# Kernel tuning notes

Measured on AMD Instinct MI355X. Metric: run time of the kernel, lower is better.

## Reference

```python
import jax, jax.numpy as jnp
import numpy as np

N_NODES = 50000
N_EDGES = 800000
F_IN = 128
F_OUT = 64
ALPHA = 0.2  # LeakyReLU negative slope


def setup_inputs() -> dict:
    key = jax.random.key(0)
    k1, k2, k3, k4, k5, k6 = jax.random.split(key, 6)
    inp = jax.random.normal(k1, (N_NODES, F_IN), dtype=jnp.float32)
    W = jax.random.normal(k2, (F_IN, F_OUT), dtype=jnp.float32) * 0.05
    a = jax.random.normal(k3, (1, 2 * F_OUT), dtype=jnp.float32) * 0.05
    adj_vals = jax.random.uniform(k4, (N_EDGES,), dtype=jnp.float32)
    src = jax.random.randint(k5, (N_EDGES,), 0, N_NODES)
    dst = jax.random.randint(k6, (N_EDGES,), 0, N_NODES)
    edge_index = jnp.stack([src, dst], axis=0).astype(jnp.int64)
    return {"input": inp, "W": W, "a": a, "adj_vals": adj_vals, "edge_index": edge_index}


def reference(input, W, a, adj_vals, edge_index):
    N = input.shape[0]
    src, dst = edge_index[0], edge_index[1]
    # h = input @ W  (dropout is identity in eval mode)
    h = input @ W  # (N, F_OUT)
    # a.mm(edge_h) with edge_h = [h[src]; h[dst]] decomposes into two per-node dots
    a_src, a_dst = a[0, :F_OUT], a[0, F_OUT:]
    score_src = h @ a_src  # (N,)
    score_dst = h @ a_dst  # (N,)
    scores = score_src[src] + score_dst[dst]  # (E,)
    edge_e = jnp.exp(-jax.nn.leaky_relu(scores, ALPHA)) * adj_vals  # (E,)
    # sparse spmm: row-sum normalizer and weighted aggregation over neighbors
    e_rowsum = jax.ops.segment_sum(edge_e, src, num_segments=N)  # (N,)
    h_prime = jax.ops.segment_sum(edge_e[:, None] * h[dst], src, num_segments=N)  # (N, F_OUT)
    h_prime = h_prime / e_rowsum[:, None]
    return jax.nn.elu(h_prime)  # concat=True
```

## Files before the change

### kernel.cpp

```cpp
#include <hip/hip_runtime.h>
#include <math.h>

#define N_NODES 50000
#define N_EDGES 800000
#define F_IN    128
#define F_OUT   64
#define ALPHA   0.2f

#define NP      50176
#define NB      196

__global__ __launch_bounds__(256) void k_gemm_scores(
    const float* __restrict__ in, const float* __restrict__ W,
    const float* __restrict__ a, float* __restrict__ h,
    float* __restrict__ ssrc, float* __restrict__ sdst) {
  __shared__ float Wl[F_IN * F_OUT];
  __shared__ float al[2 * F_OUT];

  for (int i = threadIdx.x; i < F_IN * F_OUT; i += 256) Wl[i] = W[i];
  if (threadIdx.x < 2 * F_OUT) al[threadIdx.x] = a[threadIdx.x];
  __syncthreads();

  const int wave = threadIdx.x >> 6;
  const int lane = threadIdx.x & 63;
  const int wgrp = blockIdx.x * 4 + wave;
  if (wgrp >= N_NODES / 8) return;
  const int row0 = wgrp * 8;

  const float* rb = in + (size_t)row0 * F_IN;
  float acc[8] = {0.f, 0.f, 0.f, 0.f, 0.f, 0.f, 0.f, 0.f};

  #pragma unroll 4
  for (int k4 = 0; k4 < F_IN / 4; ++k4) {
    float4 iv[8];
    #pragma unroll
    for (int r = 0; r < 8; ++r)
      iv[r] = *reinterpret_cast<const float4*>(rb + (size_t)r * F_IN + k4 * 4);
    #pragma unroll
    for (int j = 0; j < 4; ++j) {
      const float w = Wl[(k4 * 4 + j) * F_OUT + lane];
      #pragma unroll
      for (int r = 0; r < 8; ++r)
        acc[r] += (&iv[r].x)[j] * w;
    }
  }

  #pragma unroll
  for (int r = 0; r < 8; ++r)
    h[(size_t)(row0 + r) * F_OUT + lane] = acc[r];

  const float as = al[lane], ad = al[F_OUT + lane];
  float ts[8], td[8];
  #pragma unroll
  for (int r = 0; r < 8; ++r) { ts[r] = acc[r] * as; td[r] = acc[r] * ad; }
  #pragma unroll
  for (int off = 32; off; off >>= 1) {
    #pragma unroll
    for (int r = 0; r < 8; ++r) {
      ts[r] += __shfl_xor(ts[r], off);
      td[r] += __shfl_xor(td[r], off);
    }
  }
  if (lane == 0) {
    #pragma unroll
    for (int r = 0; r < 8; ++r) {
      ssrc[row0 + r] = ts[r];
      sdst[row0 + r] = td[r];
    }
  }
}

__global__ __launch_bounds__(256) void k_hist(const int* __restrict__ src,
                                              int* __restrict__ deg) {
  const int e = blockIdx.x * 256 + threadIdx.x;
  atomicAdd(&deg[src[e]], 1);
}

__global__ __launch_bounds__(256) void k_scan_a(const int* __restrict__ deg,
                                                int* __restrict__ offs,
                                                int* __restrict__ bsum) {
  __shared__ int lds[256];
  const int i = blockIdx.x * 256 + threadIdx.x;
  const int v = deg[i];
  lds[threadIdx.x] = v;
  __syncthreads();
  #pragma unroll
  for (int off = 1; off < 256; off <<= 1) {
    int t = (threadIdx.x >= off) ? lds[threadIdx.x - off] : 0;
    __syncthreads();
    lds[threadIdx.x] += t;
    __syncthreads();
  }
  offs[i] = lds[threadIdx.x] - v;
  if (threadIdx.x == 255) bsum[blockIdx.x] = lds[255];
}

__global__ __launch_bounds__(256) void k_scan_b(const int* __restrict__ bsum,
                                                int* __restrict__ boff) {
  __shared__ int lds[256];
  const int v = (threadIdx.x < NB) ? bsum[threadIdx.x] : 0;
  lds[threadIdx.x] = v;
  __syncthreads();
  #pragma unroll
  for (int off = 1; off < 256; off <<= 1) {
    int t = (threadIdx.x >= off) ? lds[threadIdx.x - off] : 0;
    __syncthreads();
    lds[threadIdx.x] += t;
    __syncthreads();
  }
  boff[threadIdx.x] = lds[threadIdx.x] - v;
}

__global__ __launch_bounds__(256) void k_scatter(
    const int* __restrict__ src, const int* __restrict__ dst,
    const float* __restrict__ adj,
    const float* __restrict__ ssrc, const float* __restrict__ sdst,
    const int* __restrict__ offs, const int* __restrict__ boff,
    int* __restrict__ cursor, int2* __restrict__ pairs) {
  const int e = blockIdx.x * 256 + threadIdx.x;
  const int s = src[e];
  const int d = dst[e];
  const float sc = ssrc[s] + sdst[d];
  const float lr = sc > 0.f ? sc : ALPHA * sc;
  const float ee = expf(-lr) * adj[e];
  const int base = offs[s] + boff[s >> 8];
  const int pos  = base + atomicAdd(&cursor[s], 1);
  pairs[pos] = make_int2(d, __float_as_int(ee));
}

__global__ __launch_bounds__(256) void k_gather(
    const int2* __restrict__ pairs, const int* __restrict__ offs,
    const int* __restrict__ boff, const float* __restrict__ h,
    float* __restrict__ out) {
  const int wave = threadIdx.x >> 6;
  const int lane = threadIdx.x & 63;
  const int node = blockIdx.x * 4 + wave;

  const int o0 = offs[node] + boff[node >> 8];
  const int o1 = offs[node + 1] + boff[(node + 1) >> 8];

  float acc = 0.f, rs = 0.f;
  int j = o0;
  for (; j + 3 < o1; j += 4) {
    const int2 p0 = pairs[j];
    const int2 p1 = pairs[j + 1];
    const int2 p2 = pairs[j + 2];
    const int2 p3 = pairs[j + 3];
    const float h0 = h[(size_t)p0.x * F_OUT + lane];
    const float h1 = h[(size_t)p1.x * F_OUT + lane];
    const float h2 = h[(size_t)p2.x * F_OUT + lane];
    const float h3 = h[(size_t)p3.x * F_OUT + lane];
    const float e0 = __int_as_float(p0.y);
    const float e1 = __int_as_float(p1.y);
    const float e2 = __int_as_float(p2.y);
    const float e3 = __int_as_float(p3.y);
    acc += e0 * h0; rs += e0;
    acc += e1 * h1; rs += e1;
    acc += e2 * h2; rs += e2;
    acc += e3 * h3; rs += e3;
  }
  for (; j < o1; ++j) {
    const int2 p = pairs[j];
    const float ee = __int_as_float(p.y);
    acc += ee * h[(size_t)p.x * F_OUT + lane];
    rs  += ee;
  }

  float v = acc / rs;
  v = v > 0.f ? v : expm1f(v);
  out[(size_t)node * F_OUT + lane] = v;
}

extern "C" void kernel_launch(void* const* d_in, const int* in_sizes, int n_in,
                              void* d_out, int out_size, void* d_ws, size_t ws_size,
                              hipStream_t stream) {
  const float* input = (const float*)d_in[0];
  const float* W     = (const float*)d_in[1];
  const float* a     = (const float*)d_in[2];
  const float* adj   = (const float*)d_in[3];
  const int*   ei    = (const int*)d_in[4];
  const int*   src   = ei;
  const int*   dst   = ei + N_EDGES;
  float* out = (float*)d_out;

  float* h    = (float*)d_ws;
  float* ssrc = h + (size_t)N_NODES * F_OUT;
  float* sdst = ssrc + N_NODES;
  int*   deg    = (int*)(sdst + N_NODES);
  int*   cursor = deg + NP;
  int*   offs   = cursor + NP;
  int*   bsum   = offs + NP;
  int*   boff   = bsum + 256;
  int2*  pairs  = (int2*)(boff + 256);

  hipMemsetAsync(deg, 0, 2 * NP * sizeof(int), stream);

  k_hist   <<<N_EDGES / 256, 256, 0, stream>>>(src, deg);
  k_scan_a <<<NB, 256, 0, stream>>>(deg, offs, bsum);
  k_scan_b <<<1, 256, 0, stream>>>(bsum, boff);
  k_gemm_scores<<<(N_NODES / 8 + 3) / 4, 256, 0, stream>>>(input, W, a, h, ssrc, sdst);
  k_scatter<<<N_EDGES / 256, 256, 0, stream>>>(src, dst, adj, ssrc, sdst,
                                               offs, boff, cursor, pairs);
  k_gather <<<N_NODES / 4, 256, 0, stream>>>(pairs, offs, boff, h, out);
}
```

Before: 260.7 us.

## Compute one node row per thread with transposed W read via broadcast loads

The GEMM now has each thread own one full input row (32 float4 held in registers) and compute all 64 outputs and both attention scores itself, which removes the LDS staging of W and the cross-lane shuffle reductions. W is transposed into workspace by an extra block added to the histogram kernel, so every lane reads the same W address (a uniform, cache-friendly broadcast). The cost is heavy register use (128 floats for the row), which lowers occupancy, and only 196 blocks are launched. Each thread also reads a strided 512-byte row, which makes input loads uncoalesced.

```diff
diff --git a/kernel.cpp b/kernel.cpp
--- a/kernel.cpp
+++ b/kernel.cpp
@@ -11,67 +11,67 @@
 #define NB      196
 
 __global__ __launch_bounds__(256) void k_gemm_scores(
-    const float* __restrict__ in, const float* __restrict__ W,
+    const float* __restrict__ in, const float* __restrict__ Wt,
     const float* __restrict__ a, float* __restrict__ h,
     float* __restrict__ ssrc, float* __restrict__ sdst) {
-  __shared__ float Wl[F_IN * F_OUT];
-  __shared__ float al[2 * F_OUT];
-
-  for (int i = threadIdx.x; i < F_IN * F_OUT; i += 256) Wl[i] = W[i];
-  if (threadIdx.x < 2 * F_OUT) al[threadIdx.x] = a[threadIdx.x];
-  __syncthreads();
-
+  const int lane = threadIdx.x & 63;
   const int wave = threadIdx.x >> 6;
-  const int lane = threadIdx.x & 63;
-  const int wgrp = blockIdx.x * 4 + wave;
-  if (wgrp >= N_NODES / 8) return;
-  const int row0 = wgrp * 8;
-
-  const float* rb = in + (size_t)row0 * F_IN;
-  float acc[8] = {0.f, 0.f, 0.f, 0.f, 0.f, 0.f, 0.f, 0.f};
-
-  #pragma unroll 4
-  for (int k4 = 0; k4 < F_IN / 4; ++k4) {
-    float4 iv[8];
+  const int row  = (blockIdx.x * 4 + wave) * 64 + lane;
+  const int rl   = row < N_NODES ? row : N_NODES - 1;
+
+  float4 ar[32];
+  const float4* rp = reinterpret_cast<const float4*>(in + (size_t)rl * F_IN);
+  #pragma unroll
+  for (int i = 0; i < 32; ++i) ar[i] = rp[i];
+
+  float ss = 0.f, sd = 0.f;
+  const bool live = (row < N_NODES);
+
+  for (int g = 0; g < 16; ++g) {
+    const float4* w0 = reinterpret_cast<const float4*>(Wt + (size_t)(g * 4 + 0) * F_IN);
+    const float4* w1 = reinterpret_cast<const float4*>(Wt + (size_t)(g * 4 + 1) * F_IN);
+    const float4* w2 = reinterpret_cast<const float4*>(Wt + (size_t)(g * 4 + 2) * F_IN);
+    const float4* w3 = reinterpret_cast<const float4*>(Wt + (size_t)(g * 4 + 3) * F_IN);
+    float a0 = 0.f, a1 = 0.f, a2 = 0.f, a3 = 0.f;
     #pragma unroll
-    for (int r = 0; r < 8; ++r)
-      iv[r] = *reinterpret_cast<const float4*>(rb + (size_t)r * F_IN + k4 * 4);
-    #pragma unroll
-    for (int j = 0; j < 4; ++j) {
-      const float w = Wl[(k4 * 4 + j) * F_OUT + lane];
-      #pragma unroll
-      for (int r = 0; r < 8; ++r)
-        acc[r] += (&iv[r].x)[j] * w;
+    for (int kb = 0; kb < 32; ++kb) {
+      const float4 r  = ar[kb];
+      const float4 v0 = w0[kb];
+      const float4 v1 = w1[kb];
+      const float4 v2 = w2[kb];
+      const float4 v3 = w3[kb];
+      a0 = fmaf(r.x, v0.x, a0); a0 = fmaf(r.y, v0.y, a0);
+      a0 = fmaf(r.z, v0.z, a0); a0 = fmaf(r.w, v0.w, a0);
+      a1 = fmaf(r.x, v1.x, a1); a1 = fmaf(r.y, v1.y, a1);
+      a1 = fmaf(r.z, v1.z, a1); a1 = fmaf(r.w, v1.w, a1);
+      a2 = fmaf(r.x, v2.x, a2); a2 = fmaf(r.y, v2.y, a2);
+      a2 = fmaf(r.z, v2.z, a2); a2 = fmaf(r.w, v2.w, a2);
+      a3 = fmaf(r.x, v3.x, a3); a3 = fmaf(r.y, v3.y, a3);
+      a3 = fmaf(r.z, v3.z, a3); a3 = fmaf(r.w, v3.w, a3);
     }
-  }
-
-  #pragma unroll
-  for (int r = 0; r < 8; ++r)
-    h[(size_t)(row0 + r) * F_OUT + lane] = acc[r];
-
-  const float as = al[lane], ad = al[F_OUT + lane];
-  float ts[8], td[8];
-  #pragma unroll
-  for (int r = 0; r < 8; ++r) { ts[r] = acc[r] * as; td[r] = acc[r] * ad; }
-  #pragma unroll
-  for (int off = 32; off; off >>= 1) {
-    #pragma unroll
-    for (int r = 0; r < 8; ++r) {
-      ts[r] += __shfl_xor(ts[r], off);
-      td[r] += __shfl_xor(td[r], off);
+    ss += a0 * a[g * 4 + 0] + a1 * a[g * 4 + 1]
+        + a2 * a[g * 4 + 2] + a3 * a[g * 4 + 3];
+    sd += a0 * a[F_OUT + g * 4 + 0] + a1 * a[F_OUT + g * 4 + 1]
+        + a2 * a[F_OUT + g * 4 + 2] + a3 * a[F_OUT + g * 4 + 3];
+    if (live) {
+      float4 hv = make_float4(a0, a1, a2, a3);
+      reinterpret_cast<float4*>(h + (size_t)row * F_OUT)[g] = hv;
     }
   }
-  if (lane == 0) {
-    #pragma unroll
-    for (int r = 0; r < 8; ++r) {
-      ssrc[row0 + r] = ts[r];
-      sdst[row0 + r] = td[r];
+  if (live) { ssrc[row] = ss; sdst[row] = sd; }
+}
+
+__global__ __launch_bounds__(256) void k_hist(const int* __restrict__ src,
+                                              int* __restrict__ deg,
+                                              const float* __restrict__ W,
+                                              float* __restrict__ Wt) {
+  if (blockIdx.x == N_EDGES / 256) {
+    for (int i = threadIdx.x; i < F_IN * F_OUT; i += 256) {
+      const int k = i >> 6, j = i & 63;
+      Wt[j * F_IN + k] = W[i];
     }
-  }
-}
-
-__global__ __launch_bounds__(256) void k_hist(const int* __restrict__ src,
-                                              int* __restrict__ deg) {
+    return;
+  }
   const int e = blockIdx.x * 256 + threadIdx.x;
   atomicAdd(&deg[src[e]], 1);
 }
@@ -191,14 +191,15 @@
   int*   offs   = cursor + NP;
   int*   bsum   = offs + NP;
   int*   boff   = bsum + 256;
-  int2*  pairs  = (int2*)(boff + 256);
+  float* Wt     = (float*)(boff + 256);
+  int2*  pairs  = (int2*)(Wt + F_IN * F_OUT);
 
   hipMemsetAsync(deg, 0, 2 * NP * sizeof(int), stream);
 
-  k_hist   <<<N_EDGES / 256, 256, 0, stream>>>(src, deg);
+  k_hist   <<<N_EDGES / 256 + 1, 256, 0, stream>>>(src, deg, W, Wt);
   k_scan_a <<<NB, 256, 0, stream>>>(deg, offs, bsum);
   k_scan_b <<<1, 256, 0, stream>>>(bsum, boff);
-  k_gemm_scores<<<(N_NODES / 8 + 3) / 4, 256, 0, stream>>>(input, W, a, h, ssrc, sdst);
+  k_gemm_scores<<<NB, 256, 0, stream>>>(input, Wt, a, h, ssrc, sdst);
   k_scatter<<<N_EDGES / 256, 256, 0, stream>>>(src, dst, adj, ssrc, sdst,
                                                offs, boff, cursor, pairs);
   k_gather <<<N_NODES / 4, 256, 0, stream>>>(pairs, offs, boff, h, out);
```

After: 303.5 us. 1.16x slower.

## Rewrite projection GEMM as 64-row LDS-tiled 4x4 register-blocked kernel

Applied to the files above, without the earlier changes.

Replaces the per-wave 8-row GEMM, in which each lane computed one output column, with a block-level 64x64 tile. The input tile is staged transposed into LDS, and each thread computes a 4x4 register block from float4 LDS reads. Score reductions now shuffle across 16 lanes. This is meant to raise arithmetic intensity and cut redundant global input loads, which the old scheme broadcast per lane. The cost is more LDS use (about 50KB per block), which may limit occupancy, and an extra sync per K-chunk.

```diff
diff --git a/kernel.cpp b/kernel.cpp
--- a/kernel.cpp
+++ b/kernel.cpp
@@ -14,58 +14,96 @@
     const float* __restrict__ in, const float* __restrict__ W,
     const float* __restrict__ a, float* __restrict__ h,
     float* __restrict__ ssrc, float* __restrict__ sdst) {
-  __shared__ float Wl[F_IN * F_OUT];
+  __shared__ float Ws[F_IN][F_OUT];
+  __shared__ float As[64][68];
   __shared__ float al[2 * F_OUT];
 
-  for (int i = threadIdx.x; i < F_IN * F_OUT; i += 256) Wl[i] = W[i];
-  if (threadIdx.x < 2 * F_OUT) al[threadIdx.x] = a[threadIdx.x];
-  __syncthreads();
-
-  const int wave = threadIdx.x >> 6;
-  const int lane = threadIdx.x & 63;
-  const int wgrp = blockIdx.x * 4 + wave;
-  if (wgrp >= N_NODES / 8) return;
-  const int row0 = wgrp * 8;
-
-  const float* rb = in + (size_t)row0 * F_IN;
-  float acc[8] = {0.f, 0.f, 0.f, 0.f, 0.f, 0.f, 0.f, 0.f};
-
-  #pragma unroll 4
-  for (int k4 = 0; k4 < F_IN / 4; ++k4) {
-    float4 iv[8];
-    #pragma unroll
-    for (int r = 0; r < 8; ++r)
-      iv[r] = *reinterpret_cast<const float4*>(rb + (size_t)r * F_IN + k4 * 4);
-    #pragma unroll
-    for (int j = 0; j < 4; ++j) {
-      const float w = Wl[(k4 * 4 + j) * F_OUT + lane];
-      #pragma unroll
-      for (int r = 0; r < 8; ++r)
-        acc[r] += (&iv[r].x)[j] * w;
-    }
-  }
-
-  #pragma unroll
-  for (int r = 0; r < 8; ++r)
-    h[(size_t)(row0 + r) * F_OUT + lane] = acc[r];
-
-  const float as = al[lane], ad = al[F_OUT + lane];
-  float ts[8], td[8];
-  #pragma unroll
-  for (int r = 0; r < 8; ++r) { ts[r] = acc[r] * as; td[r] = acc[r] * ad; }
-  #pragma unroll
-  for (int off = 32; off; off >>= 1) {
-    #pragma unroll
-    for (int r = 0; r < 8; ++r) {
-      ts[r] += __shfl_xor(ts[r], off);
-      td[r] += __shfl_xor(td[r], off);
-    }
-  }
-  if (lane == 0) {
-    #pragma unroll
-    for (int r = 0; r < 8; ++r) {
-      ssrc[row0 + r] = ts[r];
-      sdst[row0 + r] = td[r];
+  const int tid  = threadIdx.x;
+  const int row0 = blockIdx.x * 64;
+
+  {
+    const float4* Wg = reinterpret_cast<const float4*>(W);
+    float4* Wl = reinterpret_cast<float4*>(&Ws[0][0]);
+    #pragma unroll
+    for (int i = 0; i < 8; ++i) Wl[tid + i * 256] = Wg[tid + i * 256];
+  }
+  if (tid < 2 * F_OUT) al[tid] = a[tid];
+
+  const int rg = tid >> 4;
+  const int cg = tid & 15;
+  const int sr = tid >> 2;
+  const int sq = tid & 3;
+  int grow = row0 + sr; if (grow >= N_NODES) grow = N_NODES - 1;
+
+  float acc[4][4] = {{0.f}};
+
+  for (int kc = 0; kc < 2; ++kc) {
+    if (kc) __syncthreads();
+    #pragma unroll
+    for (int i = 0; i < 4; ++i) {
+      const int slot = sq + 4 * i;
+      const float4 v = *reinterpret_cast<const float4*>(
+          in + (size_t)grow * F_IN + kc * 64 + slot * 4);
+      As[slot * 4 + 0][sr] = v.x;
+      As[slot * 4 + 1][sr] = v.y;
+      As[slot * 4 + 2][sr] = v.z;
+      As[slot * 4 + 3][sr] = v.w;
+    }
+    __syncthreads();
+
+    #pragma unroll 8
+    for (int kk = 0; kk < 64; ++kk) {
+      const float4 av = *reinterpret_cast<const float4*>(&As[kk][rg * 4]);
+      const float4 bv = *reinterpret_cast<const float4*>(&Ws[kc * 64 + kk][cg * 4]);
+      acc[0][0] = fmaf(av.x, bv.x, acc[0][0]);
+      acc[0][1] = fmaf(av.x, bv.y, acc[0][1]);
+      acc[0][2] = fmaf(av.x, bv.z, acc[0][2]);
+      acc[0][3] = fmaf(av.x, bv.w, acc[0][3]);
+      acc[1][0] = fmaf(av.y, bv.x, acc[1][0]);
+      acc[1][1] = fmaf(av.y, bv.y, acc[1][1]);
+      acc[1][2] = fmaf(av.y, bv.z, acc[1][2]);
+      acc[1][3] = fmaf(av.y, bv.w, acc[1][3]);
+      acc[2][0] = fmaf(av.z, bv.x, acc[2][0]);
+      acc[2][1] = fmaf(av.z, bv.y, acc[2][1]);
+      acc[2][2] = fmaf(av.z, bv.z, acc[2][2]);
+      acc[2][3] = fmaf(av.z, bv.w, acc[2][3]);
+      acc[3][0] = fmaf(av.w, bv.x, acc[3][0]);
+      acc[3][1] = fmaf(av.w, bv.y, acc[3][1]);
+      acc[3][2] = fmaf(av.w, bv.z, acc[3][2]);
+      acc[3][3] = fmaf(av.w, bv.w, acc[3][3]);
+    }
+  }
+
+  #pragma unroll
+  for (int i = 0; i < 4; ++i) {
+    const int row = row0 + rg * 4 + i;
+    if (row < N_NODES) {
+      float4 hv = make_float4(acc[i][0], acc[i][1], acc[i][2], acc[i][3]);
+      *reinterpret_cast<float4*>(h + (size_t)row * F_OUT + cg * 4) = hv;
+    }
+  }
+
+  float ssr[4], sdr[4];
+  #pragma unroll
+  for (int i = 0; i < 4; ++i) {
+    ssr[i] = acc[i][0] * al[cg * 4 + 0] + acc[i][1] * al[cg * 4 + 1]
+           + acc[i][2] * al[cg * 4 + 2] + acc[i][3] * al[cg * 4 + 3];
+    sdr[i] = acc[i][0] * al[F_OUT + cg * 4 + 0] + acc[i][1] * al[F_OUT + cg * 4 + 1]
+           + acc[i][2] * al[F_OUT + cg * 4 + 2] + acc[i][3] * al[F_OUT + cg * 4 + 3];
+  }
+  #pragma unroll
+  for (int m = 1; m < 16; m <<= 1) {
+    #pragma unroll
+    for (int i = 0; i < 4; ++i) {
+      ssr[i] += __shfl_xor(ssr[i], m);
+      sdr[i] += __shfl_xor(sdr[i], m);
+    }
+  }
+  if (cg == 0) {
+    #pragma unroll
+    for (int i = 0; i < 4; ++i) {
+      const int row = row0 + rg * 4 + i;
+      if (row < N_NODES) { ssrc[row] = ssr[i]; sdst[row] = sdr[i]; }
     }
   }
 }
@@ -198,7 +236,7 @@
   k_hist   <<<N_EDGES / 256, 256, 0, stream>>>(src, deg);
   k_scan_a <<<NB, 256, 0, stream>>>(deg, offs, bsum);
   k_scan_b <<<1, 256, 0, stream>>>(bsum, boff);
-  k_gemm_scores<<<(N_NODES / 8 + 3) / 4, 256, 0, stream>>>(input, W, a, h, ssrc, sdst);
+  k_gemm_scores<<<(N_NODES + 63) / 64, 256, 0, stream>>>(input, W, a, h, ssrc, sdst);
   k_scatter<<<N_EDGES / 256, 256, 0, stream>>>(src, dst, adj, ssrc, sdst,
                                                offs, boff, cursor, pairs);
   k_gather <<<N_NODES / 4, 256, 0, stream>>>(pairs, offs, boff, h, out);
```

Result: faster. 216.3 us (-17.0%).
